# Performance work log

Measured on AMD Instinct MI355X. Metric: run time of the kernel, lower is better.

## Reference

```python
import jax, jax.numpy as jnp
from jax import lax
import numpy as np

INPUT = 80
H1 = 100
H2 = 50


def _lstm_layer(x, Wih, Whh, bih, bhh):
    """PyTorch-semantics single-layer LSTM, batch_first.
    x: [B,T,I]; Wih: [4H,I]; Whh: [4H,H]; biases: [4H]. Gate order: i,f,g,o.
    Returns full hidden sequence [B,T,H]."""
    B, T, _ = x.shape
    H = Whh.shape[1]
    # precompute input projections for all timesteps (one big GEMM)
    pre = jnp.einsum('bti,gi->tbg', x, Wih) + (bih + bhh)  # [T,B,4H]

    def step(carry, p):
        h, c = carry
        gates = p + h @ Whh.T  # [B,4H]
        i, f, g, o = jnp.split(gates, 4, axis=-1)
        i = jax.nn.sigmoid(i)
        f = jax.nn.sigmoid(f)
        g = jnp.tanh(g)
        o = jax.nn.sigmoid(o)
        c = f * c + i * g
        h = o * jnp.tanh(c)
        return (h, c), h

    h0 = jnp.zeros((B, H), x.dtype)
    (_, _), hs = lax.scan(step, (h0, h0), pre)  # hs: [T,B,H]
    return jnp.transpose(hs, (1, 0, 2))  # [B,T,H]


def setup_inputs() -> dict:
    key = jax.random.key(0)
    ks = jax.random.split(key, 9)
    B, T = 1024, 512
    s1 = 1.0 / np.sqrt(H1)
    s2 = 1.0 / np.sqrt(H2)
    return {
        'x': jax.random.normal(ks[0], (B, T, INPUT), dtype=jnp.float32),
        'Wih1': jax.random.uniform(ks[1], (4 * H1, INPUT), jnp.float32, -s1, s1),
        'Whh1': jax.random.uniform(ks[2], (4 * H1, H1), jnp.float32, -s1, s1),
        'bih1': jax.random.uniform(ks[3], (4 * H1,), jnp.float32, -s1, s1),
        'bhh1': jax.random.uniform(ks[4], (4 * H1,), jnp.float32, -s1, s1),
        'Wih2': jax.random.uniform(ks[5], (4 * H2, H1), jnp.float32, -s2, s2),
        'Whh2': jax.random.uniform(ks[6], (4 * H2, H2), jnp.float32, -s2, s2),
        'bih2': jax.random.uniform(ks[7], (4 * H2,), jnp.float32, -s2, s2),
        'bhh2': jax.random.uniform(ks[8], (4 * H2,), jnp.float32, -s2, s2),
    }


def reference(x, Wih1, Whh1, bih1, bhh1, Wih2, Whh2, bih2, bhh2):
    # Dropout layers are identity in eval mode.
    h1 = _lstm_layer(x, Wih1, Whh1, bih1, bhh1)   # [B,T,100]
    h2 = _lstm_layer(h1, Wih2, Whh2, bih2, bhh2)  # [B,T,50]
    return h2[:, -1, :]                            # [B,50]
```

## Files before the change

### kernel.cpp

```cpp
#include <hip/hip_runtime.h>

#define BT 1024
#define TT 512

__device__ __forceinline__ float sig_(float x) { return 1.f / (1.f + __expf(-x)); }
__device__ __forceinline__ float th_(float x)  { return 1.f - 2.f / (1.f + __expf(2.f * x)); }

template <int KS, int KPAD, int KH, int N, bool XMODE>
__device__ __forceinline__ void gp_stage(
    const float* __restrict__ A, const float* __restrict__ W,
    float (&As)[128][KPAD], float (&Bs)[KPAD][128],
    int tid, int n0, int by, int t0, int k0)
{
    constexpr int NQH = KH / 4;
#pragma unroll
    for (int ii = tid; ii < 128 * NQH; ii += 256) {
        int r = ii / NQH, q = ii % NQH;
        const float* src;
        if (XMODE) {
            int b  = (by & 7) * 128 + r;
            int tl = by >> 3;
            src = A + ((size_t)b * TT + (t0 + tl)) * KS;
        } else {
            src = A + (size_t)(by * 128 + r) * KS;
        }
        *(float4*)&As[r][q * 4] = *(const float4*)(src + k0 + q * 4);
    }
#pragma unroll
    for (int ii = tid; ii < 128 * NQH; ii += 256) {
        int n = ii & 127, kq = ii >> 7;
        float4 v = make_float4(0.f, 0.f, 0.f, 0.f);
        if (n0 + n < N) v = *(const float4*)(W + (size_t)(n0 + n) * KS + k0 + kq * 4);
        Bs[kq * 4 + 0][n] = v.x; Bs[kq * 4 + 1][n] = v.y;
        Bs[kq * 4 + 2][n] = v.z; Bs[kq * 4 + 3][n] = v.w;
    }
}

template <int KPAD, int KH>
__device__ __forceinline__ void gp_compute(
    const float (&As)[128][KPAD], const float (&Bs)[KPAD][128],
    float (&acc)[8][8], int tx, int ty)
{
    for (int kk = 0; kk < KH; kk += 4) {
        float4 bv[4][2];
#pragma unroll
        for (int r = 0; r < 4; r++) {
            bv[r][0] = *(const float4*)&Bs[kk + r][tx * 8];
            bv[r][1] = *(const float4*)&Bs[kk + r][tx * 8 + 4];
        }
#pragma unroll
        for (int i = 0; i < 8; i++) {
            float4 av = *(const float4*)&As[ty + 16 * i][kk];
#pragma unroll
            for (int s = 0; s < 2; s++) {
                acc[i][s*4+0] = fmaf(av.x, bv[0][s].x, acc[i][s*4+0]);
                acc[i][s*4+0] = fmaf(av.y, bv[1][s].x, acc[i][s*4+0]);
                acc[i][s*4+0] = fmaf(av.z, bv[2][s].x, acc[i][s*4+0]);
                acc[i][s*4+0] = fmaf(av.w, bv[3][s].x, acc[i][s*4+0]);
                acc[i][s*4+1] = fmaf(av.x, bv[0][s].y, acc[i][s*4+1]);
                acc[i][s*4+1] = fmaf(av.y, bv[1][s].y, acc[i][s*4+1]);
                acc[i][s*4+1] = fmaf(av.z, bv[2][s].y, acc[i][s*4+1]);
                acc[i][s*4+1] = fmaf(av.w, bv[3][s].y, acc[i][s*4+1]);
                acc[i][s*4+2] = fmaf(av.x, bv[0][s].z, acc[i][s*4+2]);
                acc[i][s*4+2] = fmaf(av.y, bv[1][s].z, acc[i][s*4+2]);
                acc[i][s*4+2] = fmaf(av.z, bv[2][s].z, acc[i][s*4+2]);
                acc[i][s*4+2] = fmaf(av.w, bv[3][s].z, acc[i][s*4+2]);
                acc[i][s*4+3] = fmaf(av.x, bv[0][s].w, acc[i][s*4+3]);
                acc[i][s*4+3] = fmaf(av.y, bv[1][s].w, acc[i][s*4+3]);
                acc[i][s*4+3] = fmaf(av.z, bv[2][s].w, acc[i][s*4+3]);
                acc[i][s*4+3] = fmaf(av.w, bv[3][s].w, acc[i][s*4+3]);
            }
        }
    }
}

template <int KS, int KPAD, int KH0, int N, bool XMODE>
__global__ __launch_bounds__(256, 3) void gemm_pre(
    const float* __restrict__ A, const float* __restrict__ W,
    const float* __restrict__ bih, const float* __restrict__ bhh,
    float* __restrict__ out, int t0)
{
    constexpr int KH1 = KS - KH0;
    __shared__ __align__(16) float As[128][KPAD];
    __shared__ __align__(16) float Bs[KPAD][128];
    const int tid = threadIdx.x;
    const int n0 = blockIdx.x * 128;
    const int by = blockIdx.y;
    const int Rbase = by * 128;
    const int tx = tid & 15, ty = tid >> 4;

    float acc[8][8];
#pragma unroll
    for (int i = 0; i < 8; i++)
#pragma unroll
        for (int j = 0; j < 8; j++) acc[i][j] = 0.f;

    gp_stage<KS, KPAD, KH0, N, XMODE>(A, W, As, Bs, tid, n0, by, t0, 0);
    __syncthreads();
    gp_compute<KPAD, KH0>(As, Bs, acc, tx, ty);
    __syncthreads();
    gp_stage<KS, KPAD, KH1, N, XMODE>(A, W, As, Bs, tid, n0, by, t0, KH0);
    __syncthreads();
    gp_compute<KPAD, KH1>(As, Bs, acc, tx, ty);

#pragma unroll
    for (int s = 0; s < 2; s++) {
        int n = n0 + tx * 8 + s * 4;
        if (n < N) {
            float4 bias;
            bias.x = bih[n] + bhh[n];         bias.y = bih[n + 1] + bhh[n + 1];
            bias.z = bih[n + 2] + bhh[n + 2]; bias.w = bih[n + 3] + bhh[n + 3];
#pragma unroll
            for (int i = 0; i < 8; i++) {
                size_t R = (size_t)Rbase + ty + 16 * i;
                float4 o;
                o.x = acc[i][s*4+0] + bias.x; o.y = acc[i][s*4+1] + bias.y;
                o.z = acc[i][s*4+2] + bias.z; o.w = acc[i][s*4+3] + bias.w;
                *(float4*)(out + R * N + n) = o;
            }
        }
    }
}

__global__ __launch_bounds__(1024, 2) void rec1(
    const float* __restrict__ pre,
    const float* __restrict__ Whh,
    float* __restrict__ hseq,
    float* __restrict__ cst,
    int Tc, int first)
{
    __shared__ __align__(16) float hs[4][100];
    __shared__ __align__(16) float pres[2][1600];
    __shared__ float gbuf[10 * 4 * 4 * 104];
    const int tid = threadIdx.x;
    const int b0 = blockIdx.x * 4;

    const bool comp = tid < 1000;
    const int j  = tid % 100;
    const int kq = tid / 100;

    float2 w[4][5];
    if (comp) {
#pragma unroll
        for (int g = 0; g < 4; g++) {
            const float2* W2 = (const float2*)(Whh + (size_t)(g * 100 + j) * 100 + kq * 10);
#pragma unroll
            for (int q = 0; q < 5; q++) w[g][q] = W2[q];
        }
    }

    const bool upd = tid < 400;
    const int ub = tid / 100, uj = tid % 100;
    float c = 0.f;
    if (upd) {
        float h = 0.f;
        if (!first) {
            h = hseq[((size_t)(Tc - 1) * BT + b0 + ub) * 100 + uj];
            c = cst[(size_t)(b0 + ub) * 100 + uj];
        }
        hs[ub][uj] = h;
        ((float4*)pres[0])[tid] = ((const float4*)(pre + (size_t)b0 * 400))[tid];
    }
    __syncthreads();

    int cur = 0;
    for (int t = 0; t < Tc; t++) {
        int tn = (t + 1 < Tc) ? (t + 1) : t;
        float4 pf0;
        if (upd)
            pf0 = ((const float4*)(pre + (size_t)tn * BT * 400 + (size_t)b0 * 400))[tid];

        if (comp) {
            float acc[4][4];
            const float2* h0 = (const float2*)hs[0];
            const float2* h1 = (const float2*)hs[1];
            const float2* h2 = (const float2*)hs[2];
            const float2* h3 = (const float2*)hs[3];
            {
                int f = kq * 5;
                float2 v0 = h0[f], v1 = h1[f], v2 = h2[f], v3 = h3[f];
#pragma unroll
                for (int g = 0; g < 4; g++) {
                    float2 wq = w[g][0];
                    float a0 = wq.x * v0.x; a0 = fmaf(wq.y, v0.y, a0);
                    float a1 = wq.x * v1.x; a1 = fmaf(wq.y, v1.y, a1);
                    float a2 = wq.x * v2.x; a2 = fmaf(wq.y, v2.y, a2);
                    float a3 = wq.x * v3.x; a3 = fmaf(wq.y, v3.y, a3);
                    acc[g][0] = a0; acc[g][1] = a1; acc[g][2] = a2; acc[g][3] = a3;
                }
            }
#pragma unroll
            for (int q = 1; q < 5; q++) {
                int f = kq * 5 + q;
                float2 v0 = h0[f], v1 = h1[f], v2 = h2[f], v3 = h3[f];
#pragma unroll
                for (int g = 0; g < 4; g++) {
                    float2 wq = w[g][q];
                    acc[g][0] = fmaf(wq.x, v0.x, acc[g][0]);
                    acc[g][0] = fmaf(wq.y, v0.y, acc[g][0]);
                    acc[g][1] = fmaf(wq.x, v1.x, acc[g][1]);
                    acc[g][1] = fmaf(wq.y, v1.y, acc[g][1]);
                    acc[g][2] = fmaf(wq.x, v2.x, acc[g][2]);
                    acc[g][2] = fmaf(wq.y, v2.y, acc[g][2]);
                    acc[g][3] = fmaf(wq.x, v3.x, acc[g][3]);
                    acc[g][3] = fmaf(wq.y, v3.y, acc[g][3]);
                }
            }
#pragma unroll
            for (int g = 0; g < 4; g++)
#pragma unroll
                for (int b = 0; b < 4; b++)
                    gbuf[((kq * 4 + g) * 4 + b) * 104 + j] = acc[g][b];
        }
        __syncthreads();

        if (upd) {
            const float* pb = pres[cur];
            float s0 = 0.f, s1 = 0.f, s2 = 0.f, s3 = 0.f;
#pragma unroll
            for (int q = 0; q < 10; q++) {
                int base = q * 4 * 4 * 104;
                s0 += gbuf[base + (0 * 4 + ub) * 104 + uj];
                s1 += gbuf[base + (1 * 4 + ub) * 104 + uj];
                s2 += gbuf[base + (2 * 4 + ub) * 104 + uj];
                s3 += gbuf[base + (3 * 4 + ub) * 104 + uj];
            }
            float xi = s0 + pb[ub * 400 + uj];
            float xf = s1 + pb[ub * 400 + 100 + uj];
            float xg = s2 + pb[ub * 400 + 200 + uj];
            float xo = s3 + pb[ub * 400 + 300 + uj];
            float ii = sig_(xi), ff = sig_(xf), gg = th_(xg), oo = sig_(xo);
            c = ff * c + ii * gg;
            float h = oo * th_(c);
            hs[ub][uj] = h;
            hseq[((size_t)t * BT + b0 + ub) * 100 + uj] = h;
            ((float4*)pres[cur ^ 1])[tid] = pf0;
        }
        __syncthreads();
        cur ^= 1;
    }
    if (upd) cst[(size_t)(b0 + ub) * 100 + uj] = c;
}

__global__ __launch_bounds__(256, 4) void rec2(
    const float* __restrict__ pre2,
    const float* __restrict__ Whh,
    float* __restrict__ cst, float* __restrict__ hst,
    float* __restrict__ out,
    int Tc, int first)
{
    __shared__ __align__(16) float hs[2][50];
    __shared__ __align__(16) float pres[2][400];
    __shared__ float gbuf[5 * 4 * 2 * 50];
    const int tid = threadIdx.x;
    const int b0 = blockIdx.x * 2;

    const bool comp = tid < 250;
    const int j  = tid % 50;
    const int kq = tid / 50;

    float2 w[4][5];
    if (comp) {
#pragma unroll
        for (int g = 0; g < 4; g++) {
            const float2* W2 = (const float2*)(Whh + (size_t)(g * 50 + j) * 50);
#pragma unroll
            for (int q = 0; q < 5; q++) w[g][q] = W2[kq * 5 + q];
        }
    }

    const bool upd = tid < 100;
    const int ub = tid / 50, uj = tid % 50;
    float c = 0.f, hlast = 0.f;
    if (upd) {
        float h = 0.f;
        if (!first) {
            h = hst[(size_t)(b0 + ub) * 50 + uj];
            c = cst[(size_t)(b0 + ub) * 50 + uj];
        }
        hs[ub][uj] = h;
        hlast = h;
        ((float4*)pres[0])[tid] = ((const float4*)(pre2 + (size_t)b0 * 200))[tid];
    }
    __syncthreads();

    int cur = 0;
    for (int t = 0; t < Tc; t++) {
        int tn = (t + 1 < Tc) ? (t + 1) : t;
        float4 pf0;
        if (upd)
            pf0 = ((const float4*)(pre2 + (size_t)tn * BT * 200 + (size_t)b0 * 200))[tid];

        if (comp) {
            float acc[4][2];
#pragma unroll
            for (int g = 0; g < 4; g++) { acc[g][0] = 0.f; acc[g][1] = 0.f; }
            const float2* hA = (const float2*)hs[0];
            const float2* hB = (const float2*)hs[1];
#pragma unroll
            for (int q = 0; q < 5; q++) {
                int f = kq * 5 + q;
                float2 v0 = hA[f], v1 = hB[f];
#pragma unroll
                for (int g = 0; g < 4; g++) {
                    float2 wq = w[g][q];
                    acc[g][0] = fmaf(wq.x, v0.x, acc[g][0]);
                    acc[g][0] = fmaf(wq.y, v0.y, acc[g][0]);
                    acc[g][1] = fmaf(wq.x, v1.x, acc[g][1]);
                    acc[g][1] = fmaf(wq.y, v1.y, acc[g][1]);
                }
            }
#pragma unroll
            for (int g = 0; g < 4; g++) {
                gbuf[((kq * 4 + g) * 2 + 0) * 50 + j] = acc[g][0];
                gbuf[((kq * 4 + g) * 2 + 1) * 50 + j] = acc[g][1];
            }
        }
        __syncthreads();

        if (upd) {
            const float* pb = pres[cur];
            float s0 = 0.f, s1 = 0.f, s2 = 0.f, s3 = 0.f;
#pragma unroll
            for (int q = 0; q < 5; q++) {
                int base = q * 400;
                s0 += gbuf[base + (0 * 2 + ub) * 50 + uj];
                s1 += gbuf[base + (1 * 2 + ub) * 50 + uj];
                s2 += gbuf[base + (2 * 2 + ub) * 50 + uj];
                s3 += gbuf[base + (3 * 2 + ub) * 50 + uj];
            }
            float xi = s0 + pb[ub * 200 + uj];
            float xf = s1 + pb[ub * 200 + 50 + uj];
            float xg = s2 + pb[ub * 200 + 100 + uj];
            float xo = s3 + pb[ub * 200 + 150 + uj];
            float ii = sig_(xi), ff = sig_(xf), gg = th_(xg), oo = sig_(xo);
            c = ff * c + ii * gg;
            float h = oo * th_(c);
            hs[ub][uj] = h;
            hlast = h;
            ((float4*)pres[cur ^ 1])[tid] = pf0;
        }
        __syncthreads();
        cur ^= 1;
    }
    if (upd) {
        cst[(size_t)(b0 + ub) * 50 + uj] = c;
        hst[(size_t)(b0 + ub) * 50 + uj] = hlast;
        out[(size_t)(b0 + ub) * 50 + uj] = hlast;
    }
}

extern "C" void kernel_launch(void* const* d_in, const int* in_sizes, int n_in,
                              void* d_out, int out_size, void* d_ws, size_t ws_size,
                              hipStream_t stream)
{
    const float* x    = (const float*)d_in[0];
    const float* Wih1 = (const float*)d_in[1];
    const float* Whh1 = (const float*)d_in[2];
    const float* bih1 = (const float*)d_in[3];
    const float* bhh1 = (const float*)d_in[4];
    const float* Wih2 = (const float*)d_in[5];
    const float* Whh2 = (const float*)d_in[6];
    const float* bih2 = (const float*)d_in[7];
    const float* bhh2 = (const float*)d_in[8];
    float* out = (float*)d_out;
    float* ws  = (float*)d_ws;

    int Tc = 64;
    auto need = [](int tc) -> size_t {
        return ((size_t)tc * 1024 * (400 + 100 + 200) +
                (size_t)1024 * 100 + (size_t)1024 * 50 * 2) * sizeof(float);
    };
    while (Tc > 1 && need(Tc) > ws_size) Tc >>= 1;

    float* pre1 = ws;
    float* h1s  = pre1 + (size_t)Tc * 1024 * 400;
    float* pre2 = h1s  + (size_t)Tc * 1024 * 100;
    float* c1   = pre2 + (size_t)Tc * 1024 * 200;
    float* c2   = c1 + 1024 * 100;
    float* h2st = c2 + 1024 * 50;

    const int nch = TT / Tc;
    for (int ch = 0; ch < nch; ch++) {
        int t0 = ch * Tc;
        gemm_pre<80, 40, 40, 400, true ><<<dim3(4, Tc * 8), 256, 0, stream>>>(
            x, Wih1, bih1, bhh1, pre1, t0);
        rec1<<<dim3(256), dim3(1024), 0, stream>>>(pre1, Whh1, h1s, c1, Tc, ch == 0 ? 1 : 0);
        gemm_pre<100, 52, 52, 200, false><<<dim3(2, Tc * 8), 256, 0, stream>>>(
            h1s, Wih2, bih2, bhh2, pre2, 0);
        rec2<<<dim3(512), dim3(256), 0, stream>>>(pre2, Whh2, c2, h2st, out, Tc, ch == 0 ? 1 : 0);
    }
}
```

Measured before the change: 2.728 ms.

## Split rec1 into 512 blocks of two batch rows with float4 weight slices

The layer-1 recurrence kernel now handles 2 batch rows per block with 512 threads instead of 4 rows with 1024 threads, and launches 512 blocks. Each compute thread holds a 20-wide float4 slice of the recurrent weights, so the reduction over 5 partial sums replaces 10. This gives more independent blocks to spread across CUs and halves the per-step reduction traffic. The cost is that every weight row is duplicated in registers across twice as many blocks, and each thread does more serial FMAs per step. The time-chunk length is also doubled to 128, which cuts the number of kernel launches if the workspace is large enough.

```diff
diff --git a/kernel.cpp b/kernel.cpp
--- a/kernel.cpp
+++ b/kernel.cpp
@@ -122,34 +122,40 @@
     }
 }
 
-__global__ __launch_bounds__(1024, 2) void rec1(
+__global__ __launch_bounds__(512, 4) void rec1(
     const float* __restrict__ pre,
     const float* __restrict__ Whh,
     float* __restrict__ hseq,
     float* __restrict__ cst,
     int Tc, int first)
 {
-    __shared__ __align__(16) float hs[4][100];
-    __shared__ __align__(16) float pres[2][1600];
-    __shared__ float gbuf[10 * 4 * 4 * 104];
+    __shared__ __align__(16) float hs[2][100];
+    __shared__ __align__(16) float pres[2][800];
+    __shared__ float gbuf[5 * 4 * 2 * 100];
     const int tid = threadIdx.x;
-    const int b0 = blockIdx.x * 4;
-
-    const bool comp = tid < 1000;
+    const int b0 = blockIdx.x * 2;
+
+    const bool comp = tid < 500;
     const int j  = tid % 100;
     const int kq = tid / 100;
 
-    float2 w[4][5];
+    float4 w[4][5];
     if (comp) {
 #pragma unroll
         for (int g = 0; g < 4; g++) {
-            const float2* W2 = (const float2*)(Whh + (size_t)(g * 100 + j) * 100 + kq * 10);
-#pragma unroll
-            for (int q = 0; q < 5; q++) w[g][q] = W2[q];
-        }
-    }
-
-    const bool upd = tid < 400;
+            const volatile float* Wv =
+                Whh + (size_t)(g * 100 + j) * 100 + kq * 20;
+#pragma unroll
+            for (int q = 0; q < 5; q++) {
+                w[g][q].x = Wv[q * 4 + 0];
+                w[g][q].y = Wv[q * 4 + 1];
+                w[g][q].z = Wv[q * 4 + 2];
+                w[g][q].w = Wv[q * 4 + 3];
+            }
+        }
+    }
+
+    const bool upd = tid < 200;
     const int ub = tid / 100, uj = tid % 100;
     float c = 0.f;
     if (upd) {
@@ -171,46 +177,33 @@
             pf0 = ((const float4*)(pre + (size_t)tn * BT * 400 + (size_t)b0 * 400))[tid];
 
         if (comp) {
-            float acc[4][4];
-            const float2* h0 = (const float2*)hs[0];
-            const float2* h1 = (const float2*)hs[1];
-            const float2* h2 = (const float2*)hs[2];
-            const float2* h3 = (const float2*)hs[3];
-            {
-                int f = kq * 5;
-                float2 v0 = h0[f], v1 = h1[f], v2 = h2[f], v3 = h3[f];
+            float acc[4][2];
+#pragma unroll
+            for (int g = 0; g < 4; g++) { acc[g][0] = 0.f; acc[g][1] = 0.f; }
+            const float4* h0 = (const float4*)hs[0];
+            const float4* h1 = (const float4*)hs[1];
+#pragma unroll
+            for (int q = 0; q < 5; q++) {
+                int f = kq * 5 + q;
+                float4 v0 = h0[f], v1 = h1[f];
 #pragma unroll
                 for (int g = 0; g < 4; g++) {
-                    float2 wq = w[g][0];
-                    float a0 = wq.x * v0.x; a0 = fmaf(wq.y, v0.y, a0);
-                    float a1 = wq.x * v1.x; a1 = fmaf(wq.y, v1.y, a1);
-                    float a2 = wq.x * v2.x; a2 = fmaf(wq.y, v2.y, a2);
-                    float a3 = wq.x * v3.x; a3 = fmaf(wq.y, v3.y, a3);
-                    acc[g][0] = a0; acc[g][1] = a1; acc[g][2] = a2; acc[g][3] = a3;
-                }
-            }
-#pragma unroll
-            for (int q = 1; q < 5; q++) {
-                int f = kq * 5 + q;
-                float2 v0 = h0[f], v1 = h1[f], v2 = h2[f], v3 = h3[f];
-#pragma unroll
-                for (int g = 0; g < 4; g++) {
-                    float2 wq = w[g][q];
+                    float4 wq = w[g][q];
                     acc[g][0] = fmaf(wq.x, v0.x, acc[g][0]);
                     acc[g][0] = fmaf(wq.y, v0.y, acc[g][0]);
+                    acc[g][0] = fmaf(wq.z, v0.z, acc[g][0]);
+                    acc[g][0] = fmaf(wq.w, v0.w, acc[g][0]);
                     acc[g][1] = fmaf(wq.x, v1.x, acc[g][1]);
                     acc[g][1] = fmaf(wq.y, v1.y, acc[g][1]);
-                    acc[g][2] = fmaf(wq.x, v2.x, acc[g][2]);
-                    acc[g][2] = fmaf(wq.y, v2.y, acc[g][2]);
-                    acc[g][3] = fmaf(wq.x, v3.x, acc[g][3]);
-                    acc[g][3] = fmaf(wq.y, v3.y, acc[g][3]);
+                    acc[g][1] = fmaf(wq.z, v1.z, acc[g][1]);
+                    acc[g][1] = fmaf(wq.w, v1.w, acc[g][1]);
                 }
             }
 #pragma unroll
-            for (int g = 0; g < 4; g++)
-#pragma unroll
-                for (int b = 0; b < 4; b++)
-                    gbuf[((kq * 4 + g) * 4 + b) * 104 + j] = acc[g][b];
+            for (int g = 0; g < 4; g++) {
+                gbuf[((kq * 4 + g) * 2 + 0) * 100 + j] = acc[g][0];
+                gbuf[((kq * 4 + g) * 2 + 1) * 100 + j] = acc[g][1];
+            }
         }
         __syncthreads();
 
@@ -218,12 +211,12 @@
             const float* pb = pres[cur];
             float s0 = 0.f, s1 = 0.f, s2 = 0.f, s3 = 0.f;
 #pragma unroll
-            for (int q = 0; q < 10; q++) {
-                int base = q * 4 * 4 * 104;
-                s0 += gbuf[base + (0 * 4 + ub) * 104 + uj];
-                s1 += gbuf[base + (1 * 4 + ub) * 104 + uj];
-                s2 += gbuf[base + (2 * 4 + ub) * 104 + uj];
-                s3 += gbuf[base + (3 * 4 + ub) * 104 + uj];
+            for (int q = 0; q < 5; q++) {
+                int base = q * 800;
+                s0 += gbuf[base + (0 * 2 + ub) * 100 + uj];
+                s1 += gbuf[base + (1 * 2 + ub) * 100 + uj];
+                s2 += gbuf[base + (2 * 2 + ub) * 100 + uj];
+                s3 += gbuf[base + (3 * 2 + ub) * 100 + uj];
             }
             float xi = s0 + pb[ub * 400 + uj];
             float xf = s1 + pb[ub * 400 + 100 + uj];
@@ -366,7 +359,7 @@
     float* out = (float*)d_out;
     float* ws  = (float*)d_ws;
 
-    int Tc = 64;
+    int Tc = 128;
     auto need = [](int tc) -> size_t {
         return ((size_t)tc * 1024 * (400 + 100 + 200) +
                 (size_t)1024 * 100 + (size_t)1024 * 50 * 2) * sizeof(float);
@@ -385,7 +378,7 @@
         int t0 = ch * Tc;
         gemm_pre<80, 40, 40, 400, true ><<<dim3(4, Tc * 8), 256, 0, stream>>>(
             x, Wih1, bih1, bhh1, pre1, t0);
-        rec1<<<dim3(256), dim3(1024), 0, stream>>>(pre1, Whh1, h1s, c1, Tc, ch == 0 ? 1 : 0);
+        rec1<<<dim3(512), dim3(512), 0, stream>>>(pre1, Whh1, h1s, c1, Tc, ch == 0 ? 1 : 0);
         gemm_pre<100, 52, 52, 200, false><<<dim3(2, Tc * 8), 256, 0, stream>>>(
             h1s, Wih2, bih2, bhh2, pre2, 0);
         rec2<<<dim3(512), dim3(256), 0, stream>>>(pre2, Whh2, c2, h2st, out, Tc, ch == 0 ? 1 : 0);
```

New measurement: 2.748 ms. Within noise of the previous version (+0.7%).
